# Kernel tuning notes

Hardware: AMD Instinct MI355X
Metric: run time of the kernel (lower is better)

The kernel has to match this reference:

```python
import jax, jax.numpy as jnp
import numpy as np

WINDOW_SIZE = 20
NEG_BIG = -1e8  # matches -10**8 in the torch mask


def band_mask(S):
    # 0 inside the sliding window |i-j| <= WINDOW_SIZE, -1e8 outside (additive mask)
    idx = jnp.arange(S)
    return jnp.where(jnp.abs(idx[:, None] - idx[None, :]) <= WINDOW_SIZE, 0.0, NEG_BIG).astype(jnp.float32)


def setup_inputs() -> dict:
    key = jax.random.key(0)
    k1, k2, k3, k4 = jax.random.split(key, 4)
    B, S, Dq, Dk = 8, 2048, 1024, 1024
    queries = jax.random.normal(k1, (B, S, Dq), dtype=jnp.float32)
    keys = jax.random.normal(k2, (B, S, Dk), dtype=jnp.float32)
    # reduce = nn.Linear(key_dim, query_dim) since key_dim >= query_dim
    lim = 1.0 / np.sqrt(Dk)
    W_reduce = jax.random.uniform(k3, (Dq, Dk), jnp.float32, -lim, lim)
    b_reduce = jax.random.uniform(k4, (Dq,), jnp.float32, -lim, lim)
    return {"queries": queries, "keys": keys, "W_reduce": W_reduce, "b_reduce": b_reduce}


def reference(queries, keys, W_reduce, b_reduce):
    # values default to the ORIGINAL keys (before dim matching)
    values = keys
    # match_dims: reduce keys to query_dim
    keys_r = jnp.einsum('bkd,qd->bkq', keys, W_reduce) + b_reduce  # [B,S,Dq]
    sims = jnp.einsum('bqd,bkd->bqk', queries, keys_r)             # [B,S,S]
    sims = sims + band_mask(queries.shape[1])                      # additive banded window mask
    weights = jax.nn.softmax(sims, axis=-1)
    return jnp.einsum('bqk,bkd->bqd', weights, values)
```

## Files before the change

kernel.cpp:

```cpp
#include <hip/hip_runtime.h>


#define BATCH 8
#define SEQ   2048
#define DIM   1024
#define WIN   20

typedef _Float16 half8  __attribute__((ext_vector_type(8)));
typedef _Float16 half4v __attribute__((ext_vector_type(4)));
typedef float    f32x4  __attribute__((ext_vector_type(4)));

#define GLOAD_LDS16(gsrc, ldst)                                                        \
    __builtin_amdgcn_global_load_lds(                                                  \
        (const __attribute__((address_space(1))) void*)(gsrc),                         \
        (__attribute__((address_space(3))) void*)(ldst), 16, 0, 0)

__global__ __launch_bounds__(256) void cvt_q_f16(const float* __restrict__ in,
                                                 _Float16* __restrict__ out) {
    const int n8 = (BATCH * SEQ * DIM) / 8;
    for (int i = blockIdx.x * 256 + threadIdx.x; i < n8; i += gridDim.x * 256) {
        const float4 a = ((const float4*)in)[2 * i];
        const float4 b = ((const float4*)in)[2 * i + 1];
        half8 h;
        h[0] = (_Float16)a.x; h[1] = (_Float16)a.y; h[2] = (_Float16)a.z; h[3] = (_Float16)a.w;
        h[4] = (_Float16)b.x; h[5] = (_Float16)b.y; h[6] = (_Float16)b.z; h[7] = (_Float16)b.w;
        ((half8*)out)[i] = h;
    }
}

#define WTS 68
__global__ __launch_bounds__(256) void cvt_w_t(const float* __restrict__ W,
                                               _Float16* __restrict__ WT) {
    __shared__ _Float16 tile[64 * WTS];
    const int k0 = blockIdx.x * 64;
    const int n0 = blockIdx.y * 64;
    const int t  = threadIdx.x;
    const int r  = t >> 4;
    const int c4 = (t & 15) * 4;
    #pragma unroll
    for (int rr = 0; rr < 64; rr += 16) {
        float4 v = *(const float4*)&W[(size_t)(k0 + rr + r) * DIM + n0 + c4];
        _Float16* dst = &tile[(rr + r) * WTS + c4];
        dst[0] = (_Float16)v.x; dst[1] = (_Float16)v.y;
        dst[2] = (_Float16)v.z; dst[3] = (_Float16)v.w;
    }
    __syncthreads();
    #pragma unroll
    for (int rr = 0; rr < 64; rr += 16) {
        const int n = rr + r;
        half4v h = { tile[(c4 + 0) * WTS + n], tile[(c4 + 1) * WTS + n],
                     tile[(c4 + 2) * WTS + n], tile[(c4 + 3) * WTS + n] };
        *(half4v*)&WT[(size_t)(n0 + n) * DIM + k0 + c4] = h;
    }
}

#define GK 64
__global__ __launch_bounds__(256, 2) void gemm_f16t(const _Float16* __restrict__ A,
                                                    const _Float16* __restrict__ B,
                                                    _Float16* __restrict__ C) {
    __shared__ _Float16 As[128 * GK];
    __shared__ _Float16 Bs[128 * GK];

    const int m0   = blockIdx.y * 128;
    const int n0   = blockIdx.x * 128;
    const int t    = threadIdx.x;
    const int lane = t & 63;
    const int wv   = t >> 6;
    const int wm   = (wv >> 1) * 64;
    const int wn   = (wv & 1) * 64;
    const int l15  = lane & 15;
    const int quad = lane >> 4;

    const int srow = lane >> 3;
    const int sck  = (lane & 7) ^ srow;

    f32x4 acc[4][4] = {};

    for (int k0 = 0; k0 < DIM; k0 += GK) {
        __syncthreads();
        #pragma unroll
        for (int j = 0; j < 4; ++j) {
            const int rs = (j * 4 + wv) * 8;
            GLOAD_LDS16(A + (size_t)(m0 + rs + srow) * DIM + k0 + sck * 8, &As[rs * GK]);
            GLOAD_LDS16(B + (size_t)(n0 + rs + srow) * DIM + k0 + sck * 8, &Bs[rs * GK]);
        }
        __syncthreads();

        #pragma unroll
        for (int s = 0; s < 2; ++s) {
            half8 af[4], bf[4];
            #pragma unroll
            for (int i = 0; i < 4; ++i)
                af[i] = *(const half8*)&As[(wm + i * 16 + l15) * GK +
                                           (((s * 4 + quad) ^ (l15 & 7)) * 8)];
            #pragma unroll
            for (int j = 0; j < 4; ++j)
                bf[j] = *(const half8*)&Bs[(wn + j * 16 + l15) * GK +
                                           (((s * 4 + quad) ^ (l15 & 7)) * 8)];
            #pragma unroll
            for (int i = 0; i < 4; ++i)
                #pragma unroll
                for (int j = 0; j < 4; ++j)
                    acc[i][j] = __builtin_amdgcn_mfma_f32_16x16x32_f16(af[i], bf[j], acc[i][j], 0, 0, 0);
        }
    }

    #pragma unroll
    for (int i = 0; i < 4; ++i) {
        #pragma unroll
        for (int r = 0; r < 4; ++r) {
            _Float16* crow = C + (size_t)(m0 + wm + i * 16 + quad * 4 + r) * DIM + n0 + wn + l15;
            #pragma unroll
            for (int j = 0; j < 4; ++j)
                crow[j * 16] = (_Float16)acc[i][j][r];
        }
    }
}

#define TQV  32
#define KPV  80
#define KLD2 80
#define QLD2 80
#define SLD2 84

__global__ __launch_bounds__(512, 4) void attn_v4(const _Float16* __restrict__ QT,
                                                  const float* __restrict__ Keys,
                                                  float* __restrict__ Out) {
    const int blk  = blockIdx.x;
    const int b    = blk & 7;
    const int tile = blk >> 3;
    const int q0   = tile * TQV;
    const int t    = threadIdx.x;
    const int lane = t & 63;
    const int wv   = t >> 6;
    const int l15  = lane & 15;
    const int quad = lane >> 4;

    const int klo = (q0 - WIN) > 0 ? (q0 - WIN) : 0;
    const int khi = (q0 + TQV - 1 + WIN) < (SEQ - 1) ? (q0 + TQV - 1 + WIN) : (SEQ - 1);
    const int nk  = khi - klo + 1;

    const float* keys = Keys + (size_t)b * SEQ * DIM;

    __shared__ _Float16 Qc[TQV * QLD2];
    __shared__ _Float16 Ks[KPV * KLD2];
    __shared__ float    Sl[TQV * SLD2];
    __shared__ float    Wl[TQV * SLD2];

    const int qr = t >> 4;
    const int qc = (t & 15) * 4;
    const int kr = t >> 3;
    const int kc = (t & 7) * 8;
    const int krow0 = (klo + kr) < (SEQ - 1) ? (klo + kr) : (SEQ - 1);
    const int kr2   = 64 + (t >> 3);
    const int krow2 = (klo + kr2) < (SEQ - 1) ? (klo + kr2) : (SEQ - 1);

    const _Float16* qsrc = QT + ((size_t)b * SEQ + q0 + qr) * DIM + qc;
    const float*    ksrc0 = keys + (size_t)krow0 * DIM + kc;
    const float*    ksrc2 = keys + (size_t)krow2 * DIM + kc;

    const int qt_w = wv >> 2;
    const int kt_a = wv & 3;
    const bool two = (kt_a == 0);

    f32x4 acc0 = {}, acc1 = {};

    for (int d0 = 0; d0 < DIM; d0 += 64) {
        half4v hq = *(const half4v*)(qsrc + d0);
        float4 kv0 = *(const float4*)(ksrc0 + d0);
        float4 kv1 = *(const float4*)(ksrc0 + d0 + 4);
        float4 kv2, kv3;
        if (t < 128) {
            kv2 = *(const float4*)(ksrc2 + d0);
            kv3 = *(const float4*)(ksrc2 + d0 + 4);
        }

        __syncthreads();

        *(half4v*)&Qc[qr * QLD2 + qc] = hq;
        half8 h0;
        h0[0] = (_Float16)kv0.x; h0[1] = (_Float16)kv0.y;
        h0[2] = (_Float16)kv0.z; h0[3] = (_Float16)kv0.w;
        h0[4] = (_Float16)kv1.x; h0[5] = (_Float16)kv1.y;
        h0[6] = (_Float16)kv1.z; h0[7] = (_Float16)kv1.w;
        *(half8*)&Ks[kr * KLD2 + kc] = h0;
        if (t < 128) {
            half8 h2;
            h2[0] = (_Float16)kv2.x; h2[1] = (_Float16)kv2.y;
            h2[2] = (_Float16)kv2.z; h2[3] = (_Float16)kv2.w;
            h2[4] = (_Float16)kv3.x; h2[5] = (_Float16)kv3.y;
            h2[6] = (_Float16)kv3.z; h2[7] = (_Float16)kv3.w;
            *(half8*)&Ks[kr2 * KLD2 + kc] = h2;
        }

        __syncthreads();

        #pragma unroll
        for (int s = 0; s < 2; ++s) {
            half8 af = *(const half8*)&Qc[(qt_w * 16 + l15) * QLD2 + s * 32 + quad * 8];
            half8 bf0 = *(const half8*)&Ks[(kt_a * 16 + l15) * KLD2 + s * 32 + quad * 8];
            acc0 = __builtin_amdgcn_mfma_f32_16x16x32_f16(af, bf0, acc0, 0, 0, 0);
            if (two) {
                half8 bf1 = *(const half8*)&Ks[(4 * 16 + l15) * KLD2 + s * 32 + quad * 8];
                acc1 = __builtin_amdgcn_mfma_f32_16x16x32_f16(af, bf1, acc1, 0, 0, 0);
            }
        }
    }

    __syncthreads();
    #pragma unroll
    for (int r = 0; r < 4; ++r) {
        const int q = qt_w * 16 + quad * 4 + r;
        {
            const int c = kt_a * 16 + l15;
            const int d = (q0 + q) - (klo + c);
            const bool valid = (c < nk) && ((unsigned)(d + WIN) <= 2u * WIN);
            Sl[q * SLD2 + c] = valid ? acc0[r] : -1e30f;
        }
        if (two) {
            const int c = 64 + l15;
            const int d = (q0 + q) - (klo + c);
            const bool valid = (c < nk) && ((unsigned)(d + WIN) <= 2u * WIN);
            Sl[q * SLD2 + c] = valid ? acc1[r] : -1e30f;
        }
    }
    __syncthreads();

    if (t < 128) {
        const int q = t >> 2, part = t & 3;
        const float* srow = &Sl[q * SLD2 + part * 20];
        float*       wrow = &Wl[q * SLD2 + part * 20];
        float m = -1e30f;
        #pragma unroll
        for (int i = 0; i < 20; ++i) m = fmaxf(m, srow[i]);
        m = fmaxf(m, __shfl_xor(m, 1));
        m = fmaxf(m, __shfl_xor(m, 2));
        float ssum = 0.f;
        #pragma unroll
        for (int i = 0; i < 20; ++i) { float e = expf(srow[i] - m); wrow[i] = e; ssum += e; }
        ssum += __shfl_xor(ssum, 1);
        ssum += __shfl_xor(ssum, 2);
        const float inv = 1.f / ssum;
        #pragma unroll
        for (int i = 0; i < 20; ++i) wrow[i] *= inv;
    }
    __syncthreads();

    float2 accs[TQV] = {};
    int c = 0;
    for (; c + 1 < nk; c += 2) {
        const float* ka = keys + (size_t)(klo + c) * DIM;
        const float* kb = keys + (size_t)(klo + c + 1) * DIM;
        const float a0 = ka[t], a1 = ka[t + 512];
        const float b0 = kb[t], b1 = kb[t + 512];
        #pragma unroll
        for (int q = 0; q < TQV; ++q) {
            const float2 w = *(const float2*)&Wl[q * SLD2 + c];
            accs[q].x = fmaf(w.x, a0, fmaf(w.y, b0, accs[q].x));
            accs[q].y = fmaf(w.x, a1, fmaf(w.y, b1, accs[q].y));
        }
    }
    if (c < nk) {
        const float* ka = keys + (size_t)(klo + c) * DIM;
        const float a0 = ka[t], a1 = ka[t + 512];
        #pragma unroll
        for (int q = 0; q < TQV; ++q) {
            const float w = Wl[q * SLD2 + c];
            accs[q].x = fmaf(w, a0, accs[q].x);
            accs[q].y = fmaf(w, a1, accs[q].y);
        }
    }
    #pragma unroll
    for (int q = 0; q < TQV; ++q) {
        float* orow = Out + ((size_t)b * SEQ + q0 + q) * DIM;
        orow[t]       = accs[q].x;
        orow[t + 512] = accs[q].y;
    }
}

#define LDK 40
__global__ __launch_bounds__(256) void gemm_qw_f16(const float* __restrict__ Q,
                                                   const float* __restrict__ W,
                                                   float* __restrict__ QT) {
    __shared__ _Float16 Asl[128 * LDK];
    __shared__ _Float16 Bsl[128 * LDK];

    const int m0 = blockIdx.x * 128;
    const int n0 = blockIdx.y * 128;
    const int t  = threadIdx.x;
    const int lane = t & 63;
    const int wv   = t >> 6;
    const int wm   = (wv >> 1) * 64;
    const int wn   = (wv & 1) * 64;
    const int l15  = lane & 15;
    const int quad = lane >> 4;

    const int ar = t >> 1;
    const int ac = (t & 1) * 16;
    const float* Aptr = Q + (size_t)(m0 + ar) * DIM + ac;
    _Float16* AsW = &Asl[ar * LDK + ac];

    const int br = t >> 3;
    const int bc = t & 7;
    const float* Bptr = W + (size_t)br * DIM + n0 + bc;

    f32x4 acc[4][4] = {};

    for (int k0 = 0; k0 < DIM; k0 += 32) {
        float4 a0 = *(const float4*)(Aptr + k0);
        float4 a1 = *(const float4*)(Aptr + k0 + 4);
        float4 a2 = *(const float4*)(Aptr + k0 + 8);
        float4 a3 = *(const float4*)(Aptr + k0 + 12);
        float bv[16];
        #pragma unroll
        for (int j = 0; j < 16; ++j) bv[j] = Bptr[(size_t)k0 * DIM + 8 * j];

        __syncthreads();

        half8 h0, h1;
        h0[0] = (_Float16)a0.x; h0[1] = (_Float16)a0.y; h0[2] = (_Float16)a0.z; h0[3] = (_Float16)a0.w;
        h0[4] = (_Float16)a1.x; h0[5] = (_Float16)a1.y; h0[6] = (_Float16)a1.z; h0[7] = (_Float16)a1.w;
        h1[0] = (_Float16)a2.x; h1[1] = (_Float16)a2.y; h1[2] = (_Float16)a2.z; h1[3] = (_Float16)a2.w;
        h1[4] = (_Float16)a3.x; h1[5] = (_Float16)a3.y; h1[6] = (_Float16)a3.z; h1[7] = (_Float16)a3.w;
        *(half8*)(AsW)     = h0;
        *(half8*)(AsW + 8) = h1;

        #pragma unroll
        for (int j = 0; j < 16; ++j)
            Bsl[(bc + 8 * j) * LDK + br] = (_Float16)bv[j];

        __syncthreads();

        half8 af[4], bf[4];
        #pragma unroll
        for (int i = 0; i < 4; ++i)
            af[i] = *(const half8*)&Asl[(wm + i * 16 + l15) * LDK + quad * 8];
        #pragma unroll
        for (int j = 0; j < 4; ++j)
            bf[j] = *(const half8*)&Bsl[(wn + j * 16 + l15) * LDK + quad * 8];

        #pragma unroll
        for (int i = 0; i < 4; ++i)
            #pragma unroll
            for (int j = 0; j < 4; ++j)
                acc[i][j] = __builtin_amdgcn_mfma_f32_16x16x32_f16(af[i], bf[j], acc[i][j], 0, 0, 0);
    }

    #pragma unroll
    for (int i = 0; i < 4; ++i) {
        const int row0 = m0 + wm + i * 16 + quad * 4;
        #pragma unroll
        for (int r = 0; r < 4; ++r) {
            float* orow = QT + (size_t)(row0 + r) * DIM + n0 + wn + l15;
            #pragma unroll
            for (int j = 0; j < 4; ++j)
                orow[j * 16] = acc[i][j][r];
        }
    }
}

#define TQ  16
#define KP  64
#define KLD 80
#define QLD 80
#define SLD 66

__global__ __launch_bounds__(256, 4) void attn_fb(const float* __restrict__ QT,
                                                  const float* __restrict__ Keys,
                                                  float* __restrict__ Out) {
    const int blk  = blockIdx.x;
    const int b    = blk & 7;
    const int tile = blk >> 3;
    const int q0   = tile * TQ;
    const int t    = threadIdx.x;
    const int lane = t & 63;
    const int wv   = t >> 6;
    const int l15  = lane & 15;
    const int quad = lane >> 4;

    const int klo = (q0 - WIN) > 0 ? (q0 - WIN) : 0;
    const int khi = (q0 + TQ - 1 + WIN) < (SEQ - 1) ? (q0 + TQ - 1 + WIN) : (SEQ - 1);
    const int nk  = khi - klo + 1;

    const float* qt   = QT + ((size_t)b * SEQ + q0) * DIM;
    const float* keys = Keys + (size_t)b * SEQ * DIM;

    __shared__ _Float16 Qc[TQ * QLD];
    __shared__ _Float16 Ks[KP * KLD];
    __shared__ float    Sl[TQ * SLD];
    __shared__ float    Wl[TQ * SLD];

    const int qr = t >> 4;
    const int qc = (t & 15) * 4;
    const int kr = t >> 2;
    const int kc = (t & 3) * 4;
    const int krow = (klo + kr) < (SEQ - 1) ? (klo + kr) : (SEQ - 1);

    const float* qsrc = qt + (size_t)qr * DIM + qc;
    const float* ksrc = keys + (size_t)krow * DIM + kc;

    f32x4 acc_s = {};

    for (int d0 = 0; d0 < DIM; d0 += 64) {
        const float4 qv = *(const float4*)(qsrc + d0);
        float4 kv0 = *(const float4*)(ksrc + d0);
        float4 kv1 = *(const float4*)(ksrc + d0 + 16);
        float4 kv2 = *(const float4*)(ksrc + d0 + 32);
        float4 kv3 = *(const float4*)(ksrc + d0 + 48);

        __syncthreads();

        half4v hq = {(_Float16)qv.x, (_Float16)qv.y, (_Float16)qv.z, (_Float16)qv.w};
        *(half4v*)&Qc[qr * QLD + qc] = hq;
        half4v h0 = {(_Float16)kv0.x, (_Float16)kv0.y, (_Float16)kv0.z, (_Float16)kv0.w};
        half4v h1 = {(_Float16)kv1.x, (_Float16)kv1.y, (_Float16)kv1.z, (_Float16)kv1.w};
        half4v h2 = {(_Float16)kv2.x, (_Float16)kv2.y, (_Float16)kv2.z, (_Float16)kv2.w};
        half4v h3 = {(_Float16)kv3.x, (_Float16)kv3.y, (_Float16)kv3.z, (_Float16)kv3.w};
        *(half4v*)&Ks[kr * KLD + kc]      = h0;
        *(half4v*)&Ks[kr * KLD + kc + 16] = h1;
        *(half4v*)&Ks[kr * KLD + kc + 32] = h2;
        *(half4v*)&Ks[kr * KLD + kc + 48] = h3;

        __syncthreads();

        #pragma unroll
        for (int s = 0; s < 2; ++s) {
            half8 af = *(const half8*)&Qc[l15 * QLD + s * 32 + quad * 8];
            half8 bf = *(const half8*)&Ks[(wv * 16 + l15) * KLD + s * 32 + quad * 8];
            acc_s = __builtin_amdgcn_mfma_f32_16x16x32_f16(af, bf, acc_s, 0, 0, 0);
        }
    }

    __syncthreads();
    #pragma unroll
    for (int r = 0; r < 4; ++r) {
        const int q = quad * 4 + r;
        const int c = wv * 16 + l15;
        const int d = (q0 + q) - (klo + c);
        const bool valid = (c < nk) && ((unsigned)(d + WIN) <= 2u * WIN);
        Sl[q * SLD + c] = valid ? acc_s[r] : -1e30f;
    }
    __syncthreads();

    if (t < 64) {
        const int q = t >> 2, part = t & 3;
        const float* srow = &Sl[q * SLD + part * 16];
        float*       wrow = &Wl[q * SLD + part * 16];
        float m = -1e30f;
        #pragma unroll
        for (int i = 0; i < 16; ++i) m = fmaxf(m, srow[i]);
        m = fmaxf(m, __shfl_xor(m, 1));
        m = fmaxf(m, __shfl_xor(m, 2));
        float ssum = 0.f;
        #pragma unroll
        for (int i = 0; i < 16; ++i) { float e = expf(srow[i] - m); wrow[i] = e; ssum += e; }
        ssum += __shfl_xor(ssum, 1);
        ssum += __shfl_xor(ssum, 2);
        const float inv = 1.f / ssum;
        #pragma unroll
        for (int i = 0; i < 16; ++i) wrow[i] *= inv;
    }
    __syncthreads();

    float accs[TQ][4] = {};
    for (int c = 0; c < nk; ++c) {
        const float* krow2 = keys + (size_t)(klo + c) * DIM;
        const float k0 = krow2[t], k1 = krow2[t + 256], k2 = krow2[t + 512], k3 = krow2[t + 768];
        #pragma unroll
        for (int q = 0; q < TQ; ++q) {
            const float w = Wl[q * SLD + c];
            accs[q][0] = fmaf(w, k0, accs[q][0]);
            accs[q][1] = fmaf(w, k1, accs[q][1]);
            accs[q][2] = fmaf(w, k2, accs[q][2]);
            accs[q][3] = fmaf(w, k3, accs[q][3]);
        }
    }
    #pragma unroll
    for (int q = 0; q < TQ; ++q) {
        float* orow = Out + ((size_t)b * SEQ + q0 + q) * DIM;
        orow[t]       = accs[q][0];
        orow[t + 256] = accs[q][1];
        orow[t + 512] = accs[q][2];
        orow[t + 768] = accs[q][3];
    }
}

extern "C" void kernel_launch(void* const* d_in, const int* in_sizes, int n_in,
                              void* d_out, int out_size, void* d_ws, size_t ws_size,
                              hipStream_t stream) {
    const float* queries = (const float*)d_in[0];
    const float* keys    = (const float*)d_in[1];
    const float* W       = (const float*)d_in[2];
    float* out = (float*)d_out;

    const size_t qt16_bytes = (size_t)BATCH * SEQ * DIM * sizeof(_Float16);
    const size_t w16_bytes  = (size_t)DIM * DIM * sizeof(_Float16);

    if (ws_size >= qt16_bytes + w16_bytes) {
        _Float16* q16  = (_Float16*)d_out;
        _Float16* qt16 = (_Float16*)d_ws;
        _Float16* w16t = (_Float16*)((char*)d_ws + qt16_bytes);

        cvt_q_f16<<<2048, 256, 0, stream>>>(queries, q16);
        cvt_w_t<<<dim3(16, 16), 256, 0, stream>>>(W, w16t);
        gemm_f16t<<<dim3(8, 128), 256, 0, stream>>>(q16, w16t, qt16);
        const int nblk = (BATCH * SEQ) / TQV;
        attn_v4<<<nblk, 512, 0, stream>>>(qt16, keys, out);
    } else {
        gemm_qw_f16<<<dim3(128, 8), 256, 0, stream>>>(queries, W, out);
        const int nblk = (BATCH * SEQ) / TQ;
        attn_fb<<<nblk, 256, 0, stream>>>(out, keys, out);
    }
}
```

Measured before the change: 279.0 us.

## Compute attention P·V with fp16 MFMA over LDS-staged value chunks

Replaces the scalar FMA loop that multiplies softmax weights by fp32 values read directly from global memory with an MFMA path. Softmax weights are written as fp16 into a zero-padded LDS tile, and value rows are staged per 64-column chunk into LDS as fp16. Each wave then accumulates a 16x16 output tile with 16x16x32 f16 MFMAs. This trades fp32 value precision for fp16 and adds two barriers per chunk, strided scalar LDS reads for the B fragment, and narrow 64-byte output stores.

```diff
diff --git a/kernel.cpp b/kernel.cpp
--- a/kernel.cpp
+++ b/kernel.cpp
@@ -118,12 +118,13 @@
 }
 
 #define TQV  32
-#define KPV  80
+#define KSR  96
 #define KLD2 80
 #define QLD2 80
 #define SLD2 84
-
-__global__ __launch_bounds__(512, 4) void attn_v4(const _Float16* __restrict__ QT,
+#define PLD  104
+
+__global__ __launch_bounds__(512, 4) void attn_v5(const _Float16* __restrict__ QT,
                                                   const float* __restrict__ Keys,
                                                   float* __restrict__ Out) {
     const int blk  = blockIdx.x;
@@ -143,9 +144,9 @@
     const float* keys = Keys + (size_t)b * SEQ * DIM;
 
     __shared__ _Float16 Qc[TQV * QLD2];
-    __shared__ _Float16 Ks[KPV * KLD2];
+    __shared__ _Float16 Ks[KSR * KLD2];
     __shared__ float    Sl[TQV * SLD2];
-    __shared__ float    Wl[TQV * SLD2];
+    __shared__ _Float16 Pl[TQV * PLD];
 
     const int qr = t >> 4;
     const int qc = (t & 15) * 4;
@@ -155,7 +156,7 @@
     const int kr2   = 64 + (t >> 3);
     const int krow2 = (klo + kr2) < (SEQ - 1) ? (klo + kr2) : (SEQ - 1);
 
-    const _Float16* qsrc = QT + ((size_t)b * SEQ + q0 + qr) * DIM + qc;
+    const _Float16* qsrc  = QT + ((size_t)b * SEQ + q0 + qr) * DIM + qc;
     const float*    ksrc0 = keys + (size_t)krow0 * DIM + kc;
     const float*    ksrc2 = keys + (size_t)krow2 * DIM + kc;
 
@@ -229,52 +230,75 @@
     if (t < 128) {
         const int q = t >> 2, part = t & 3;
         const float* srow = &Sl[q * SLD2 + part * 20];
-        float*       wrow = &Wl[q * SLD2 + part * 20];
+        _Float16*    prow = &Pl[q * PLD + part * 20];
         float m = -1e30f;
+        float e[20];
         #pragma unroll
         for (int i = 0; i < 20; ++i) m = fmaxf(m, srow[i]);
         m = fmaxf(m, __shfl_xor(m, 1));
         m = fmaxf(m, __shfl_xor(m, 2));
         float ssum = 0.f;
         #pragma unroll
-        for (int i = 0; i < 20; ++i) { float e = expf(srow[i] - m); wrow[i] = e; ssum += e; }
+        for (int i = 0; i < 20; ++i) { e[i] = expf(srow[i] - m); ssum += e[i]; }
         ssum += __shfl_xor(ssum, 1);
         ssum += __shfl_xor(ssum, 2);
         const float inv = 1.f / ssum;
         #pragma unroll
-        for (int i = 0; i < 20; ++i) wrow[i] *= inv;
-    }
-    __syncthreads();
-
-    float2 accs[TQV] = {};
-    int c = 0;
-    for (; c + 1 < nk; c += 2) {
-        const float* ka = keys + (size_t)(klo + c) * DIM;
-        const float* kb = keys + (size_t)(klo + c + 1) * DIM;
-        const float a0 = ka[t], a1 = ka[t + 512];
-        const float b0 = kb[t], b1 = kb[t + 512];
-        #pragma unroll
-        for (int q = 0; q < TQV; ++q) {
-            const float2 w = *(const float2*)&Wl[q * SLD2 + c];
-            accs[q].x = fmaf(w.x, a0, fmaf(w.y, b0, accs[q].x));
-            accs[q].y = fmaf(w.x, a1, fmaf(w.y, b1, accs[q].y));
-        }
-    }
-    if (c < nk) {
-        const float* ka = keys + (size_t)(klo + c) * DIM;
-        const float a0 = ka[t], a1 = ka[t + 512];
-        #pragma unroll
-        for (int q = 0; q < TQV; ++q) {
-            const float w = Wl[q * SLD2 + c];
-            accs[q].x = fmaf(w, a0, accs[q].x);
-            accs[q].y = fmaf(w, a1, accs[q].y);
-        }
-    }
-    #pragma unroll
-    for (int q = 0; q < TQV; ++q) {
-        float* orow = Out + ((size_t)b * SEQ + q0 + q) * DIM;
-        orow[t]       = accs[q].x;
-        orow[t + 512] = accs[q].y;
+        for (int i = 0; i < 20; ++i) prow[i] = (_Float16)(e[i] * inv);
+        if (part == 3) {
+            #pragma unroll
+            for (int i = 0; i < 16; ++i) Pl[q * PLD + 80 + i] = (_Float16)0.f;
+        }
+    }
+    __syncthreads();
+
+    const int dt_w = wv & 3;
+    const int kr2b  = 64 + (t >> 3);
+    const int krow2b = (klo + kr2b) < (SEQ - 1) ? (klo + kr2b) : (SEQ - 1);
+    const float* ksrc2b = keys + (size_t)krow2b * DIM + kc;
+
+    for (int ch = 0; ch < 16; ++ch) {
+        const int d0 = ch * 64;
+        float4 kv0 = *(const float4*)(ksrc0 + d0);
+        float4 kv1 = *(const float4*)(ksrc0 + d0 + 4);
+        float4 kv2, kv3;
+        if (t < 256) {
+            kv2 = *(const float4*)(ksrc2b + d0);
+            kv3 = *(const float4*)(ksrc2b + d0 + 4);
+        }
+
+        __syncthreads();
+
+        half8 h0;
+        h0[0] = (_Float16)kv0.x; h0[1] = (_Float16)kv0.y;
+        h0[2] = (_Float16)kv0.z; h0[3] = (_Float16)kv0.w;
+        h0[4] = (_Float16)kv1.x; h0[5] = (_Float16)kv1.y;
+        h0[6] = (_Float16)kv1.z; h0[7] = (_Float16)kv1.w;
+        *(half8*)&Ks[kr * KLD2 + kc] = h0;
+        if (t < 256) {
+            half8 h2;
+            h2[0] = (_Float16)kv2.x; h2[1] = (_Float16)kv2.y;
+            h2[2] = (_Float16)kv2.z; h2[3] = (_Float16)kv2.w;
+            h2[4] = (_Float16)kv3.x; h2[5] = (_Float16)kv3.y;
+            h2[6] = (_Float16)kv3.z; h2[7] = (_Float16)kv3.w;
+            *(half8*)&Ks[kr2b * KLD2 + kc] = h2;
+        }
+
+        __syncthreads();
+
+        f32x4 accO = {};
+        #pragma unroll
+        for (int s = 0; s < 3; ++s) {
+            half8 af = *(const half8*)&Pl[(qt_w * 16 + l15) * PLD + s * 32 + quad * 8];
+            half8 bf;
+            #pragma unroll
+            for (int j = 0; j < 8; ++j)
+                bf[j] = Ks[(s * 32 + quad * 8 + j) * KLD2 + dt_w * 16 + l15];
+            accO = __builtin_amdgcn_mfma_f32_16x16x32_f16(af, bf, accO, 0, 0, 0);
+        }
+        #pragma unroll
+        for (int r = 0; r < 4; ++r)
+            Out[((size_t)b * SEQ + q0 + qt_w * 16 + quad * 4 + r) * DIM + d0 + dt_w * 16 + l15] = accO[r];
     }
 }
 
@@ -505,7 +529,7 @@
         cvt_w_t<<<dim3(16, 16), 256, 0, stream>>>(W, w16t);
         gemm_f16t<<<dim3(8, 128), 256, 0, stream>>>(q16, w16t, qt16);
         const int nblk = (BATCH * SEQ) / TQV;
-        attn_v4<<<nblk, 512, 0, stream>>>(qt16, keys, out);
+        attn_v5<<<nblk, 512, 0, stream>>>(qt16, keys, out);
     } else {
         gemm_qw_f16<<<dim3(128, 8), 256, 0, stream>>>(queries, W, out);
         const int nblk = (BATCH * SEQ) / TQ;
```

Measured after the change: 251.2 us. 10.0% less time.
